# Kernel tuning notes

Measured on AMD Instinct MI355X. Metric: run time of the kernel, lower is better.

The kernel has to match this reference:

```python
import jax, jax.numpy as jnp
import numpy as np

B, S, D, H = 2, 2048, 1024, 16
HD = D // H
SCALE = HD ** -0.5
NEG = -1e30


def setup_inputs() -> dict:
    key = jax.random.key(0)
    ks = jax.random.split(key, 10)
    w = lambda k: jax.random.normal(k, (D, D), dtype=jnp.float32) * 0.02
    b = lambda k: jax.random.normal(k, (D,), dtype=jnp.float32) * 0.01
    hidden_states = jax.random.normal(ks[0], (B, S, D), dtype=jnp.float32)
    document_ids = jnp.sort(jax.random.randint(ks[1], (S,), 0, 16))
    return {
        'hidden_states': hidden_states,
        'wq': w(ks[2]), 'bq': b(ks[3]),
        'wk': w(ks[4]), 'bk': b(ks[5]),
        'wv': w(ks[6]), 'bv': b(ks[7]),
        'wo': w(ks[8]), 'bo': b(ks[9]),
        'document_ids': document_ids,
    }


def reference(hidden_states, wq, bq, wk, bk, wv, bv, wo, bo, document_ids):
    # projections (nn.Linear: x @ W.T + b)
    q = (hidden_states @ wq.T + bq).reshape(B, S, H, HD)
    k = (hidden_states @ wk.T + bk).reshape(B, S, H, HD)
    v = (hidden_states @ wv.T + bv).reshape(B, S, H, HD)
    # document-block mask: attend only within same document
    mask = document_ids[:, None] == document_ids[None, :]  # [S, S]
    scores = jnp.einsum('bqhd,bkhd->bhqk', q, k) * SCALE
    scores = jnp.where(mask[None, None], scores, NEG)
    attn = jax.nn.softmax(scores, axis=-1)
    out = jnp.einsum('bhqk,bkhd->bqhd', attn, v).reshape(B, S, D)
    return out @ wo.T + bo
```

## Files before the change

kernel.cpp:

```cpp
#include <hip/hip_runtime.h>
#include <hip/hip_bf16.h>
#include <math.h>

#define B 2
#define S 2048
#define D 1024
#define H 16
#define HD 64
#define SCALE 0.125f
#define NEGBIG -1e30f

#define NE 4194304
#define NW 1048576
#define NE8 524288
#define NW8 131072

typedef _Float16 f16;
typedef _Float16 f16x8 __attribute__((ext_vector_type(8)));
typedef _Float16 f16x4 __attribute__((ext_vector_type(4)));
typedef float f32x4  __attribute__((ext_vector_type(4)));

__device__ __forceinline__ void gl_lds16(const void* g, void* l) {
    __builtin_amdgcn_global_load_lds(
        (const __attribute__((address_space(1))) unsigned int*)g,
        (__attribute__((address_space(3))) unsigned int*)l, 16, 0, 0);
}

__device__ __forceinline__ void wave_lds_fence() {
    __builtin_amdgcn_wave_barrier();
    __builtin_amdgcn_s_waitcnt(0xC07F);
    __builtin_amdgcn_wave_barrier();
}

__global__ __launch_bounds__(256) void prep_k(
    const float4* __restrict__ hs,
    const float4* __restrict__ wq, const float4* __restrict__ wk,
    const float4* __restrict__ wv, const float4* __restrict__ wo,
    const int* __restrict__ doc,
    f16x8* __restrict__ xh, f16x8* __restrict__ wqkv, f16x8* __restrict__ woh,
    int* __restrict__ dstart, int* __restrict__ dend)
{
    int i = blockIdx.x * blockDim.x + threadIdx.x;
    if (i < NE8 + 4 * NW8) {
        const float4* src;
        f16x8* dst;
        if (i < NE8) { src = hs + 2 * (size_t)i; dst = xh + i; }
        else {
            int j = i - NE8;
            int id = j / NW8, jj = j - id * NW8;
            src = ((id == 0) ? wq : (id == 1) ? wk : (id == 2) ? wv : wo) + 2 * (size_t)jj;
            dst = (id < 3) ? (wqkv + (size_t)id * NW8 + jj) : (woh + jj);
        }
        float4 a = src[0], b = src[1];
        f16x8 h;
        h[0] = (f16)a.x; h[1] = (f16)a.y; h[2] = (f16)a.z; h[3] = (f16)a.w;
        h[4] = (f16)b.x; h[5] = (f16)b.y; h[6] = (f16)b.z; h[7] = (f16)b.w;
        *dst = h;
    } else {
        int s = i - (NE8 + 4 * NW8);
        if (s < S) {
            int v = doc[s];
            int lo = 0, hi = S;
            while (lo < hi) { int mid = (lo + hi) >> 1; if (doc[mid] < v) lo = mid + 1; else hi = mid; }
            dstart[s] = lo;
            lo = 0; hi = S;
            while (lo < hi) { int mid = (lo + hi) >> 1; if (doc[mid] <= v) lo = mid + 1; else hi = mid; }
            dend[s] = lo;
        }
    }
}

__global__ __launch_bounds__(256) void qkv_mfma_k(
    const f16* __restrict__ xh, const f16* __restrict__ wqkv,
    const float* __restrict__ bq, const float* __restrict__ bk,
    const float* __restrict__ bv,
    f16* __restrict__ Qh, f16* __restrict__ Kh, f16* __restrict__ Vth)
{
    __shared__ union {
        struct { f16 Ah[128 * 32]; f16 Bh[128 * 32]; } s;
        f16 tr[64 * 136];
    } lds;

    const int which = blockIdx.z;
    const f16* Bhg = wqkv + (size_t)which * D * D;

    const int tid = threadIdx.x;
    const int w = tid >> 6, ln = tid & 63;
    const int wm = (w & 1) * 64, wn = (w >> 1) * 64;
    const int lc = ln & 15, quad = ln >> 4;
    const int srow = ln >> 2, slot = ln & 3;
    const int m0 = blockIdx.y * 128, n0 = blockIdx.x * 128;

    int a_off[4], b_off[4];
    #pragma unroll
    for (int t = 0; t < 4; t++) {
        int am = wm + t * 16 + lc;
        a_off[t] = am * 32 + ((quad ^ ((am >> 1) & 3)) * 8);
        int bn = wn + t * 16 + lc;
        b_off[t] = bn * 32 + ((quad ^ ((bn >> 1) & 3)) * 8);
    }

    f32x4 acc[4][4];
    #pragma unroll
    for (int i = 0; i < 4; i++)
        #pragma unroll
        for (int j = 0; j < 4; j++) acc[i][j] = (f32x4){0.f, 0.f, 0.f, 0.f};

    for (int k0 = 0; k0 < 1024; k0 += 32) {
        #pragma unroll
        for (int half = 0; half < 2; half++) {
            int rl = half * 64 + w * 16 + srow;
            int q = slot ^ ((rl >> 1) & 3);
            size_t ga = (size_t)(m0 + rl) * 1024 + k0 + q * 8;
            size_t gb = (size_t)(n0 + rl) * 1024 + k0 + q * 8;
            int lofs = (half * 64 + w * 16) * 32;
            gl_lds16(xh + ga, lds.s.Ah + lofs);
            gl_lds16(Bhg + gb, lds.s.Bh + lofs);
        }
        __syncthreads();

        f16x8 ah[4], bh[4];
        #pragma unroll
        for (int t = 0; t < 4; t++) {
            ah[t] = *(const f16x8*)&lds.s.Ah[a_off[t]];
            bh[t] = *(const f16x8*)&lds.s.Bh[b_off[t]];
        }
        #pragma unroll
        for (int mt = 0; mt < 4; mt++)
            #pragma unroll
            for (int nt = 0; nt < 4; nt++)
                acc[mt][nt] = __builtin_amdgcn_mfma_f32_16x16x32_f16(ah[mt], bh[nt], acc[mt][nt], 0, 0, 0);
        __syncthreads();
    }

    if (which < 2) {
        const float* bias = (which == 0) ? bq : bk;
        #pragma unroll
        for (int nt = 0; nt < 4; nt++) {
            int col = n0 + wn + nt * 16 + lc;
            float bv_ = bias[col];
            int h = col >> 6, hd = col & 63;
            #pragma unroll
            for (int mt = 0; mt < 4; mt++) {
                #pragma unroll
                for (int r = 0; r < 4; r++) {
                    int m = m0 + wm + mt * 16 + quad * 4 + r;
                    int bbm = m >> 11, s = m & (S - 1);
                    float val = acc[mt][nt][r] + bv_;
                    if (which == 0) val *= SCALE;
                    size_t idx = (((size_t)(bbm * H + h) * S) + s) * HD + hd;
                    ((which == 0) ? Qh : Kh)[idx] = (f16)val;
                }
            }
        }
    } else {
        const int bb = m0 >> 11;
        const int sbase = m0 & (S - 1);
        #pragma unroll
        for (int pass = 0; pass < 2; pass++) {
            if ((w >> 1) == pass) {
                #pragma unroll
                for (int nt = 0; nt < 4; nt++) {
                    int colp = nt * 16 + lc;
                    float bv_ = bv[n0 + pass * 64 + colp];
                    #pragma unroll
                    for (int mt = 0; mt < 4; mt++) {
                        f16x4 v;
                        #pragma unroll
                        for (int r = 0; r < 4; r++) v[r] = (f16)(acc[mt][nt][r] + bv_);
                        *(f16x4*)&lds.tr[colp * 136 + wm + mt * 16 + quad * 4] = v;
                    }
                }
            }
            __syncthreads();
            #pragma unroll
            for (int p2 = 0; p2 < 4; p2++) {
                int chunk = tid + p2 * 256;
                int colp = chunk >> 4;
                int oct = chunk & 15;
                f16x8 v = *(const f16x8*)&lds.tr[colp * 136 + oct * 8];
                int vcol = n0 + pass * 64 + colp;
                int h = vcol >> 6, hd = vcol & 63;
                size_t idx = (((size_t)(bb * H + h) * HD) + hd) * S + sbase + oct * 8;
                *(f16x8*)(Vth + idx) = v;
            }
            __syncthreads();
        }
    }
}

__global__ __launch_bounds__(256) void out_mfma_k(
    const f16* __restrict__ oh, const f16* __restrict__ wh,
    const float* __restrict__ bias, float* __restrict__ Y)
{
    __shared__ f16 Ah[128 * 32], Bh[128 * 32];
    const int tid = threadIdx.x;
    const int w = tid >> 6, ln = tid & 63;
    const int wm = (w & 1) * 64, wn = (w >> 1) * 64;
    const int lc = ln & 15, quad = ln >> 4;
    const int srow = ln >> 2, slot = ln & 3;
    const int m0 = blockIdx.y * 128, n0 = blockIdx.x * 128;

    int a_off[4], b_off[4];
    #pragma unroll
    for (int t = 0; t < 4; t++) {
        int am = wm + t * 16 + lc;
        a_off[t] = am * 32 + ((quad ^ ((am >> 1) & 3)) * 8);
        int bn = wn + t * 16 + lc;
        b_off[t] = bn * 32 + ((quad ^ ((bn >> 1) & 3)) * 8);
    }

    f32x4 acc[4][4];
    #pragma unroll
    for (int i = 0; i < 4; i++)
        #pragma unroll
        for (int j = 0; j < 4; j++) acc[i][j] = (f32x4){0.f, 0.f, 0.f, 0.f};

    for (int k0 = 0; k0 < 1024; k0 += 32) {
        #pragma unroll
        for (int half = 0; half < 2; half++) {
            int rl = half * 64 + w * 16 + srow;
            int q = slot ^ ((rl >> 1) & 3);
            size_t ga = (size_t)(m0 + rl) * 1024 + k0 + q * 8;
            size_t gb = (size_t)(n0 + rl) * 1024 + k0 + q * 8;
            int lofs = (half * 64 + w * 16) * 32;
            gl_lds16(oh + ga, Ah + lofs);
            gl_lds16(wh + gb, Bh + lofs);
        }
        __syncthreads();

        f16x8 ah[4], bh[4];
        #pragma unroll
        for (int t = 0; t < 4; t++) {
            ah[t] = *(const f16x8*)&Ah[a_off[t]];
            bh[t] = *(const f16x8*)&Bh[b_off[t]];
        }
        #pragma unroll
        for (int mt = 0; mt < 4; mt++)
            #pragma unroll
            for (int nt = 0; nt < 4; nt++)
                acc[mt][nt] = __builtin_amdgcn_mfma_f32_16x16x32_f16(ah[mt], bh[nt], acc[mt][nt], 0, 0, 0);
        __syncthreads();
    }

    #pragma unroll
    for (int nt = 0; nt < 4; nt++) {
        int col = n0 + wn + nt * 16 + lc;
        float bv_ = bias[col];
        #pragma unroll
        for (int mt = 0; mt < 4; mt++) {
            #pragma unroll
            for (int r = 0; r < 4; r++) {
                int m = m0 + wm + mt * 16 + quad * 4 + r;
                Y[(size_t)m * D + col] = acc[mt][nt][r] + bv_;
            }
        }
    }
}

__global__ __launch_bounds__(256) void attn4_k(
    const f16* __restrict__ Qh, const f16* __restrict__ Kh,
    const f16* __restrict__ Vth,
    const int* __restrict__ dstart, const int* __restrict__ dend,
    f16* __restrict__ Ohi)
{
    const int qt = blockIdx.x, h = blockIdx.y, b = blockIdx.z;
    const int tid = threadIdx.x;
    const int w = tid >> 6, ln = tid & 63;
    const int lc = ln & 15, quad = ln >> 4;
    const int q0 = qt * 64 + w * 16;
    const size_t bh  = ((size_t)b * H + h) * S;
    const size_t bhv = ((size_t)b * H + h) * HD;

    __shared__ float Ps[4][2][16 * 65];

    int row_st[4], row_en[4];
    #pragma unroll
    for (int r = 0; r < 4; r++) {
        row_st[r] = dstart[q0 + quad * 4 + r];
        row_en[r] = dend[q0 + quad * 4 + r];
    }
    const int kstart = dstart[q0] & ~63;
    const int kend   = dend[q0 + 15];

    const size_t qrow = bh + q0 + lc;
    f16x8 qf[2];
    #pragma unroll
    for (int ks = 0; ks < 2; ks++)
        qf[ks] = *(const f16x8*)(Qh + qrow * HD + ks * 32 + quad * 8);

    f32x4 o[4];
    #pragma unroll
    for (int nt = 0; nt < 4; nt++) o[nt] = (f32x4){0.f, 0.f, 0.f, 0.f};
    f32x4 m_i = (f32x4){NEGBIG, NEGBIG, NEGBIG, NEGBIG};
    f32x4 l_i = (f32x4){0.f, 0.f, 0.f, 0.f};

    int it = 0;
    for (int j0 = kstart; j0 < kend; j0 += 64, it ^= 1) {
        float* ps = &Ps[w][it][0];

        f16x8 kf[4][2];
        #pragma unroll
        for (int t = 0; t < 4; t++) {
            size_t krow = (bh + j0 + t * 16 + lc) * HD;
            #pragma unroll
            for (int ks = 0; ks < 2; ks++)
                kf[t][ks] = *(const f16x8*)(Kh + krow + ks * 32 + quad * 8);
        }

        f32x4 sc[4];
        #pragma unroll
        for (int t = 0; t < 4; t++) {
            f32x4 a = (f32x4){0.f, 0.f, 0.f, 0.f};
            #pragma unroll
            for (int ks = 0; ks < 2; ks++)
                a = __builtin_amdgcn_mfma_f32_16x16x32_f16(qf[ks], kf[t][ks], a, 0, 0, 0);
            int key = j0 + t * 16 + lc;
            #pragma unroll
            for (int r = 0; r < 4; r++) {
                bool valid = (key >= row_st[r]) && (key < row_en[r]);
                sc[t][r] = valid ? a[r] : NEGBIG;
            }
        }

        f32x4 mx = sc[0];
        #pragma unroll
        for (int t = 1; t < 4; t++)
            #pragma unroll
            for (int r = 0; r < 4; r++) mx[r] = fmaxf(mx[r], sc[t][r]);
        #pragma unroll
        for (int off = 1; off <= 8; off <<= 1)
            #pragma unroll
            for (int r = 0; r < 4; r++) mx[r] = fmaxf(mx[r], __shfl_xor(mx[r], off, 64));

        f32x4 m_new, alpha;
        #pragma unroll
        for (int r = 0; r < 4; r++) {
            m_new[r] = fmaxf(m_i[r], mx[r]);
            alpha[r] = __expf(m_i[r] - m_new[r]);
        }

        f32x4 psum = (f32x4){0.f, 0.f, 0.f, 0.f};
        f32x4 pv[4];
        #pragma unroll
        for (int t = 0; t < 4; t++) {
            #pragma unroll
            for (int r = 0; r < 4; r++) {
                float p = __expf(sc[t][r] - m_new[r]);
                p = (sc[t][r] < -5e29f) ? 0.f : p;
                pv[t][r] = p;
                psum[r] += p;
            }
        }
        #pragma unroll
        for (int off = 1; off <= 8; off <<= 1)
            #pragma unroll
            for (int r = 0; r < 4; r++) psum[r] += __shfl_xor(psum[r], off, 64);

        #pragma unroll
        for (int r = 0; r < 4; r++) {
            l_i[r] = l_i[r] * alpha[r] + psum[r];
            m_i[r] = m_new[r];
        }
        #pragma unroll
        for (int nt = 0; nt < 4; nt++)
            #pragma unroll
            for (int r = 0; r < 4; r++) o[nt][r] *= alpha[r];

        #pragma unroll
        for (int t = 0; t < 4; t++) {
            int g = 2 * t + (lc >> 3);
            #pragma unroll
            for (int r = 0; r < 4; r++) {
                int q = quad * 4 + r;
                ps[q * 65 + ((g ^ (q & 7)) * 8) + (lc & 7)] = pv[t][r];
            }
        }

        wave_lds_fence();

        #pragma unroll
        for (int ks = 0; ks < 2; ks++) {
            int gp = ks * 4 + quad;
            const float* prow = &ps[lc * 65 + ((gp ^ (lc & 7)) * 8)];
            f16x8 ph;
            #pragma unroll
            for (int j = 0; j < 8; j++) ph[j] = (f16)prow[j];
            #pragma unroll
            for (int nt = 0; nt < 4; nt++) {
                int dim = nt * 16 + lc;
                f16x8 vh = *(const f16x8*)(Vth + (bhv + dim) * S + j0 + gp * 8);
                o[nt] = __builtin_amdgcn_mfma_f32_16x16x32_f16(ph, vh, o[nt], 0, 0, 0);
            }
        }
    }

    f32x4 inv;
    #pragma unroll
    for (int r = 0; r < 4; r++) inv[r] = 1.f / l_i[r];
    #pragma unroll
    for (int nt = 0; nt < 4; nt++) {
        int dim = nt * 16 + lc;
        #pragma unroll
        for (int r = 0; r < 4; r++) {
            int q = q0 + quad * 4 + r;
            float val = o[nt][r] * inv[r];
            size_t idx = ((size_t)(b * S + q)) * D + h * 64 + dim;
            Ohi[idx] = (f16)val;
        }
    }
}

extern "C" void kernel_launch(void* const* d_in, const int* in_sizes, int n_in,
                              void* d_out, int out_size, void* d_ws, size_t ws_size,
                              hipStream_t stream) {
    const float* hs = (const float*)d_in[0];
    const float* wq = (const float*)d_in[1];
    const float* bq = (const float*)d_in[2];
    const float* wk = (const float*)d_in[3];
    const float* bk = (const float*)d_in[4];
    const float* wv = (const float*)d_in[5];
    const float* bv = (const float*)d_in[6];
    const float* wo = (const float*)d_in[7];
    const float* bo = (const float*)d_in[8];
    const int*  doc = (const int*)d_in[9];
    float* out = (float*)d_out;

    f16* xh   = (f16*)d_ws;
    f16* Qhb  = xh + NE;
    f16* Khb  = Qhb + NE;
    f16* Vth  = Khb + NE;
    f16* wqkv = Vth + NE;
    f16* woh  = wqkv + 3 * (size_t)NW;
    int* dstart = (int*)(woh + NW);
    int* dend = dstart + S;

    prep_k<<<(NE8 + 4 * NW8 + S + 255) / 256, 256, 0, stream>>>(
        (const float4*)hs, (const float4*)wq, (const float4*)wk,
        (const float4*)wv, (const float4*)wo, doc,
        (f16x8*)xh, (f16x8*)wqkv, (f16x8*)woh, dstart, dend);

    qkv_mfma_k<<<dim3(D / 128, (B * S) / 128, 3), 256, 0, stream>>>(
        xh, wqkv, bq, bk, bv, Qhb, Khb, Vth);
    attn4_k<<<dim3(S / 64, H, B), 256, 0, stream>>>(
        Qhb, Khb, Vth, dstart, dend, xh);
    out_mfma_k<<<dim3(D / 128, (B * S) / 128), 256, 0, stream>>>(xh, woh, bo, out);
}
```

Baseline: 201.3 us.

## Deepen GEMM K-tiles, shrink output GEMM N-tile, prefetch K/V in attention

Both projection GEMMs now stage a K depth of 64 per iteration with an 8-way XOR swizzle, which halves the number of barrier pairs. The output GEMM also switches to a 128x64 tile so it launches twice as many blocks and fills more CUs. The attention kernel software-prefetches the next K fragment during the current block and issues the V loads before the P write/read, to hide global latency. The cost is more LDS and registers per block, which could reduce occupancy.

```diff
diff --git a/kernel.cpp b/kernel.cpp
--- a/kernel.cpp
+++ b/kernel.cpp
@@ -77,7 +77,7 @@
     f16* __restrict__ Qh, f16* __restrict__ Kh, f16* __restrict__ Vth)
 {
     __shared__ union {
-        struct { f16 Ah[128 * 32]; f16 Bh[128 * 32]; } s;
+        struct { f16 Ah[128 * 64]; f16 Bh[128 * 64]; } s;
         f16 tr[64 * 136];
     } lds;
 
@@ -88,48 +88,43 @@
     const int w = tid >> 6, ln = tid & 63;
     const int wm = (w & 1) * 64, wn = (w >> 1) * 64;
     const int lc = ln & 15, quad = ln >> 4;
-    const int srow = ln >> 2, slot = ln & 3;
     const int m0 = blockIdx.y * 128, n0 = blockIdx.x * 128;
 
-    int a_off[4], b_off[4];
-    #pragma unroll
-    for (int t = 0; t < 4; t++) {
-        int am = wm + t * 16 + lc;
-        a_off[t] = am * 32 + ((quad ^ ((am >> 1) & 3)) * 8);
-        int bn = wn + t * 16 + lc;
-        b_off[t] = bn * 32 + ((quad ^ ((bn >> 1) & 3)) * 8);
-    }
-
     f32x4 acc[4][4];
     #pragma unroll
     for (int i = 0; i < 4; i++)
         #pragma unroll
         for (int j = 0; j < 4; j++) acc[i][j] = (f32x4){0.f, 0.f, 0.f, 0.f};
 
-    for (int k0 = 0; k0 < 1024; k0 += 32) {
-        #pragma unroll
-        for (int half = 0; half < 2; half++) {
-            int rl = half * 64 + w * 16 + srow;
-            int q = slot ^ ((rl >> 1) & 3);
-            size_t ga = (size_t)(m0 + rl) * 1024 + k0 + q * 8;
-            size_t gb = (size_t)(n0 + rl) * 1024 + k0 + q * 8;
-            int lofs = (half * 64 + w * 16) * 32;
+    for (int k0 = 0; k0 < 1024; k0 += 64) {
+        #pragma unroll
+        for (int i = 0; i < 4; i++) {
+            int rl = w * 32 + i * 8 + (ln >> 3);
+            int oc = (ln & 7) ^ (rl & 7);
+            size_t ga = (size_t)(m0 + rl) * 1024 + k0 + oc * 8;
+            size_t gb = (size_t)(n0 + rl) * 1024 + k0 + oc * 8;
+            int lofs = (w * 32 + i * 8) * 64;
             gl_lds16(xh + ga, lds.s.Ah + lofs);
             gl_lds16(Bhg + gb, lds.s.Bh + lofs);
         }
         __syncthreads();
 
-        f16x8 ah[4], bh[4];
-        #pragma unroll
-        for (int t = 0; t < 4; t++) {
-            ah[t] = *(const f16x8*)&lds.s.Ah[a_off[t]];
-            bh[t] = *(const f16x8*)&lds.s.Bh[b_off[t]];
-        }
-        #pragma unroll
-        for (int mt = 0; mt < 4; mt++)
-            #pragma unroll
-            for (int nt = 0; nt < 4; nt++)
-                acc[mt][nt] = __builtin_amdgcn_mfma_f32_16x16x32_f16(ah[mt], bh[nt], acc[mt][nt], 0, 0, 0);
+        #pragma unroll
+        for (int ks = 0; ks < 2; ks++) {
+            f16x8 ah[4], bh[4];
+            #pragma unroll
+            for (int t = 0; t < 4; t++) {
+                int am = wm + t * 16 + lc;
+                ah[t] = *(const f16x8*)&lds.s.Ah[am * 64 + (((ks * 4 + quad) ^ (am & 7)) * 8)];
+                int bn = wn + t * 16 + lc;
+                bh[t] = *(const f16x8*)&lds.s.Bh[bn * 64 + (((ks * 4 + quad) ^ (bn & 7)) * 8)];
+            }
+            #pragma unroll
+            for (int mt = 0; mt < 4; mt++)
+                #pragma unroll
+                for (int nt = 0; nt < 4; nt++)
+                    acc[mt][nt] = __builtin_amdgcn_mfma_f32_16x16x32_f16(ah[mt], bh[nt], acc[mt][nt], 0, 0, 0);
+        }
         __syncthreads();
     }
 
@@ -193,58 +188,58 @@
     const f16* __restrict__ oh, const f16* __restrict__ wh,
     const float* __restrict__ bias, float* __restrict__ Y)
 {
-    __shared__ f16 Ah[128 * 32], Bh[128 * 32];
+    __shared__ f16 Ah[128 * 64], Bh[64 * 64];
     const int tid = threadIdx.x;
     const int w = tid >> 6, ln = tid & 63;
-    const int wm = (w & 1) * 64, wn = (w >> 1) * 64;
+    const int wm = (w & 1) * 64, wn = (w >> 1) * 32;
     const int lc = ln & 15, quad = ln >> 4;
-    const int srow = ln >> 2, slot = ln & 3;
-    const int m0 = blockIdx.y * 128, n0 = blockIdx.x * 128;
-
-    int a_off[4], b_off[4];
-    #pragma unroll
-    for (int t = 0; t < 4; t++) {
-        int am = wm + t * 16 + lc;
-        a_off[t] = am * 32 + ((quad ^ ((am >> 1) & 3)) * 8);
-        int bn = wn + t * 16 + lc;
-        b_off[t] = bn * 32 + ((quad ^ ((bn >> 1) & 3)) * 8);
-    }
-
-    f32x4 acc[4][4];
+    const int m0 = blockIdx.y * 128, n0 = blockIdx.x * 64;
+
+    f32x4 acc[4][2];
     #pragma unroll
     for (int i = 0; i < 4; i++)
         #pragma unroll
-        for (int j = 0; j < 4; j++) acc[i][j] = (f32x4){0.f, 0.f, 0.f, 0.f};
-
-    for (int k0 = 0; k0 < 1024; k0 += 32) {
-        #pragma unroll
-        for (int half = 0; half < 2; half++) {
-            int rl = half * 64 + w * 16 + srow;
-            int q = slot ^ ((rl >> 1) & 3);
-            size_t ga = (size_t)(m0 + rl) * 1024 + k0 + q * 8;
-            size_t gb = (size_t)(n0 + rl) * 1024 + k0 + q * 8;
-            int lofs = (half * 64 + w * 16) * 32;
-            gl_lds16(oh + ga, Ah + lofs);
-            gl_lds16(wh + gb, Bh + lofs);
+        for (int j = 0; j < 2; j++) acc[i][j] = (f32x4){0.f, 0.f, 0.f, 0.f};
+
+    for (int k0 = 0; k0 < 1024; k0 += 64) {
+        #pragma unroll
+        for (int i = 0; i < 4; i++) {
+            int rl = w * 32 + i * 8 + (ln >> 3);
+            int oc = (ln & 7) ^ (rl & 7);
+            gl_lds16(oh + (size_t)(m0 + rl) * 1024 + k0 + oc * 8, Ah + (w * 32 + i * 8) * 64);
+        }
+        #pragma unroll
+        for (int i = 0; i < 2; i++) {
+            int rl = w * 16 + i * 8 + (ln >> 3);
+            int oc = (ln & 7) ^ (rl & 7);
+            gl_lds16(wh + (size_t)(n0 + rl) * 1024 + k0 + oc * 8, Bh + (w * 16 + i * 8) * 64);
         }
         __syncthreads();
 
-        f16x8 ah[4], bh[4];
-        #pragma unroll
-        for (int t = 0; t < 4; t++) {
-            ah[t] = *(const f16x8*)&Ah[a_off[t]];
-            bh[t] = *(const f16x8*)&Bh[b_off[t]];
-        }
-        #pragma unroll
-        for (int mt = 0; mt < 4; mt++)
-            #pragma unroll
-            for (int nt = 0; nt < 4; nt++)
-                acc[mt][nt] = __builtin_amdgcn_mfma_f32_16x16x32_f16(ah[mt], bh[nt], acc[mt][nt], 0, 0, 0);
+        #pragma unroll
+        for (int ks = 0; ks < 2; ks++) {
+            f16x8 ah[4], bh[2];
+            #pragma unroll
+            for (int t = 0; t < 4; t++) {
+                int am = wm + t * 16 + lc;
+                ah[t] = *(const f16x8*)&Ah[am * 64 + (((ks * 4 + quad) ^ (am & 7)) * 8)];
+            }
+            #pragma unroll
+            for (int t = 0; t < 2; t++) {
+                int bn = wn + t * 16 + lc;
+                bh[t] = *(const f16x8*)&Bh[bn * 64 + (((ks * 4 + quad) ^ (bn & 7)) * 8)];
+            }
+            #pragma unroll
+            for (int mt = 0; mt < 4; mt++)
+                #pragma unroll
+                for (int nt = 0; nt < 2; nt++)
+                    acc[mt][nt] = __builtin_amdgcn_mfma_f32_16x16x32_f16(ah[mt], bh[nt], acc[mt][nt], 0, 0, 0);
+        }
         __syncthreads();
     }
 
     #pragma unroll
-    for (int nt = 0; nt < 4; nt++) {
+    for (int nt = 0; nt < 2; nt++) {
         int col = n0 + wn + nt * 16 + lc;
         float bv_ = bias[col];
         #pragma unroll
@@ -255,6 +250,18 @@
                 Y[(size_t)m * D + col] = acc[mt][nt][r] + bv_;
             }
         }
+    }
+}
+
+__device__ __forceinline__ void load_kfrag(
+    const f16* __restrict__ Kh, size_t bh, int j0, int lc, int quad, f16x8 kf[4][2])
+{
+    #pragma unroll
+    for (int t = 0; t < 4; t++) {
+        size_t krow = (bh + j0 + t * 16 + lc) * HD;
+        #pragma unroll
+        for (int ks = 0; ks < 2; ks++)
+            kf[t][ks] = *(const f16x8*)(Kh + krow + ks * 32 + quad * 8);
     }
 }
 
@@ -295,18 +302,14 @@
     f32x4 m_i = (f32x4){NEGBIG, NEGBIG, NEGBIG, NEGBIG};
     f32x4 l_i = (f32x4){0.f, 0.f, 0.f, 0.f};
 
+    f16x8 kf[4][2], kf2[4][2];
+    load_kfrag(Kh, bh, kstart, lc, quad, kf);
+
     int it = 0;
     for (int j0 = kstart; j0 < kend; j0 += 64, it ^= 1) {
         float* ps = &Ps[w][it][0];
-
-        f16x8 kf[4][2];
-        #pragma unroll
-        for (int t = 0; t < 4; t++) {
-            size_t krow = (bh + j0 + t * 16 + lc) * HD;
-            #pragma unroll
-            for (int ks = 0; ks < 2; ks++)
-                kf[t][ks] = *(const f16x8*)(Kh + krow + ks * 32 + quad * 8);
-        }
+        const bool more = (j0 + 64) < kend;
+        if (more) load_kfrag(Kh, bh, j0 + 64, lc, quad, kf2);
 
         f32x4 sc[4];
         #pragma unroll
@@ -367,6 +370,17 @@
             #pragma unroll
             for (int r = 0; r < 4; r++) o[nt][r] *= alpha[r];
 
+        f16x8 vh[2][4];
+        #pragma unroll
+        for (int ks = 0; ks < 2; ks++) {
+            int gp = ks * 4 + quad;
+            #pragma unroll
+            for (int nt = 0; nt < 4; nt++) {
+                int dim = nt * 16 + lc;
+                vh[ks][nt] = *(const f16x8*)(Vth + (bhv + dim) * S + j0 + gp * 8);
+            }
+        }
+
         #pragma unroll
         for (int t = 0; t < 4; t++) {
             int g = 2 * t + (lc >> 3);
@@ -387,11 +401,15 @@
             #pragma unroll
             for (int j = 0; j < 8; j++) ph[j] = (f16)prow[j];
             #pragma unroll
-            for (int nt = 0; nt < 4; nt++) {
-                int dim = nt * 16 + lc;
-                f16x8 vh = *(const f16x8*)(Vth + (bhv + dim) * S + j0 + gp * 8);
-                o[nt] = __builtin_amdgcn_mfma_f32_16x16x32_f16(ph, vh, o[nt], 0, 0, 0);
-            }
+            for (int nt = 0; nt < 4; nt++)
+                o[nt] = __builtin_amdgcn_mfma_f32_16x16x32_f16(ph, vh[ks][nt], o[nt], 0, 0, 0);
+        }
+
+        if (more) {
+            #pragma unroll
+            for (int t = 0; t < 4; t++)
+                #pragma unroll
+                for (int ks = 0; ks < 2; ks++) kf[t][ks] = kf2[t][ks];
         }
     }
 
@@ -444,5 +462,5 @@
         xh, wqkv, bq, bk, bv, Qhb, Khb, Vth);
     attn4_k<<<dim3(S / 64, H, B), 256, 0, stream>>>(
         Qhb, Khb, Vth, dstart, dend, xh);
-    out_mfma_k<<<dim3(D / 128, (B * S) / 128), 256, 0, stream>>>(xh, woh, bo, out);
-}
+    out_mfma_k<<<dim3(D / 64, (B * S) / 128), 256, 0, stream>>>(xh, woh, bo, out);
+}
```

After: 192.9 us. 1.04x faster.
